# Performance work log

Hardware: AMD Instinct MI355X
Metric: run time of the kernel (lower is better)

Reference implementation:

```python
import jax, jax.numpy as jnp
import numpy as np

IN_SIZE = 64
NUM_FEATURES = 32
NUM_HEADS = 8
EPS = 1e-5


def setup_inputs() -> dict:
    key = jax.random.key(0)
    ks = jax.random.split(key, 12)
    D, F, Hh = IN_SIZE, NUM_FEATURES, NUM_HEADS
    M = Hh * F  # MLP width = num_heads * num_features
    s = 0.05
    return {
        "x": jax.random.normal(ks[0], (2, D, 48, 48), dtype=jnp.float32),
        # stacked per-head projection weights, stored [in, out]
        "Wq": jax.random.normal(ks[1], (Hh, D, F), dtype=jnp.float32) * s,
        "bq": jax.random.normal(ks[2], (Hh, F), dtype=jnp.float32) * s,
        "Wk": jax.random.normal(ks[3], (Hh, D, F), dtype=jnp.float32) * s,
        "bk": jax.random.normal(ks[4], (Hh, F), dtype=jnp.float32) * s,
        "Wv": jax.random.normal(ks[5], (Hh, D, F), dtype=jnp.float32) * s,
        "bv": jax.random.normal(ks[6], (Hh, F), dtype=jnp.float32) * s,
        "W1": jax.random.normal(ks[7], (M, M), dtype=jnp.float32) * s,
        "b1": jax.random.normal(ks[8], (M,), dtype=jnp.float32) * s,
        "W2": jax.random.normal(ks[9], (M, M), dtype=jnp.float32) * s,
        "b2": jax.random.normal(ks[10], (M,), dtype=jnp.float32) * s,
        "gamma": jnp.ones((M,), dtype=jnp.float32),
        "beta": jnp.zeros((M,), dtype=jnp.float32),
    }


def _inorm_lastdim(y):
    # InstanceNorm1d applied to channels-last tensor: normalizes LAST dim,
    # biased variance, eps=1e-5, no affine.
    mu = jnp.mean(y, axis=-1, keepdims=True)
    var = jnp.mean(jnp.square(y - mu), axis=-1, keepdims=True)
    return (y - mu) / jnp.sqrt(var + EPS)


def reference(x, Wq, bq, Wk, bk, Wv, bv, W1, b1, W2, b2, gamma, beta):
    N, D, H, W = x.shape
    F = NUM_FEATURES
    L = H * W
    flat = jnp.transpose(x, (0, 2, 3, 1)).reshape(N, L, D)  # [N, L, D]

    def proj(Wm, bm):  # Wm [Hh, D, F], bm [Hh, F] -> [Hh, N, L, F]
        y = jnp.einsum('nld,hdf->hnlf', flat, Wm) + bm[:, None, None, :]
        return jax.nn.relu(_inorm_lastdim(y))

    Q = proj(Wq, bq)
    K = proj(Wk, bk)
    V = proj(Wv, bv)

    scores = jnp.einsum('hnlf,hnmf->hnlm', Q, K) / jnp.sqrt(jnp.float32(F))
    # original: F.softmax(scaled) on 3D [N,L,L] -> legacy dim=1 (first L axis)
    att = jax.nn.softmax(scores, axis=2)
    A = jnp.einsum('hnlm,hnmf->hnlf', att, V)  # [Hh, N, L, F]

    heads = jnp.transpose(A, (1, 2, 0, 3)).reshape(N, L, NUM_HEADS * F)
    m = jax.nn.relu(heads @ W1 + b1)
    m = jax.nn.relu(m @ W2 + b2)
    o = _inorm_lastdim(m + heads)
    o = gamma * o + beta  # [N, L, Hh*F]
    return jnp.transpose(o, (0, 2, 1)).reshape(N, NUM_HEADS * F, H, W)
```

## Files before the change

### kernel.cpp

```cpp
#include <hip/hip_runtime.h>
#include <hip/hip_bf16.h>
#include <stdint.h>

#define L_TOT 2304
#define D_IN  64
#define NF    32
#define NH    8
#define NB    2
#define MW    256
#define CHS   4
#define NSTRIP (L_TOT/32)
#define RT    32

constexpr float EPSV  = 1e-5f;
constexpr float SCALE = 0.17677669529663687f;
constexpr float SHIFT = 20.0f;

typedef __bf16  bf16x8  __attribute__((ext_vector_type(8)));
typedef float   f32x16  __attribute__((ext_vector_type(16)));

union U32x4BF { uint32_t u[4]; bf16x8 v; };

static __device__ __forceinline__ uint32_t pack_bf16(float a, float b) {
    union { __bf16 h[2]; uint32_t u; } r;
    r.h[0] = (__bf16)a;
    r.h[1] = (__bf16)b;
    return r.u;
}

__global__ void k_prep(const float* __restrict__ W1, const float* __restrict__ W2,
                       __hip_bfloat16* __restrict__ W1t, __hip_bfloat16* __restrict__ W2t)
{
    const float* src = blockIdx.z ? W2 : W1;
    __hip_bfloat16* dst = blockIdx.z ? W2t : W1t;
    __shared__ float t[32][33];
    const int bi = blockIdx.x * 32, bj = blockIdx.y * 32;
    #pragma unroll
    for (int k = 0; k < 4; ++k)
        t[threadIdx.y + 8*k][threadIdx.x] = src[(size_t)(bi + threadIdx.y + 8*k) * MW + bj + threadIdx.x];
    __syncthreads();
    #pragma unroll
    for (int k = 0; k < 4; ++k)
        dst[(size_t)(bj + threadIdx.y + 8*k) * MW + bi + threadIdx.x] =
            __float2bfloat16(t[threadIdx.x][threadIdx.y + 8*k]);
}

__global__ __launch_bounds__(256) void k_prep2(
    const float* __restrict__ x,
    const float* __restrict__ Wq, const float* __restrict__ Wk, const float* __restrict__ Wv,
    __hip_bfloat16* __restrict__ xb, __hip_bfloat16* __restrict__ Wqkvt)
{
    const int job = blockIdx.x;
    const int tx = threadIdx.x & 31, ty = threadIdx.x >> 5;
    const float* src;
    size_t sstride;
    __hip_bfloat16* dst;
    if (job < 24) {
        int mtx = job >> 3, h = job & 7;
        const float* Wm = mtx == 0 ? Wq : (mtx == 1 ? Wk : Wv);
        src = Wm + (size_t)h * D_IN * NF;
        sstride = NF;
        dst = Wqkvt + (size_t)job * NF * D_IN;
    } else {
        int i = job - 24;
        int n = i / NSTRIP, lt = i % NSTRIP;
        src = x + (size_t)n * D_IN * L_TOT + lt * 32;
        sstride = L_TOT;
        dst = xb + ((size_t)n * L_TOT + lt * 32) * D_IN;
    }
    __shared__ float t[64][33];
    #pragma unroll
    for (int k = 0; k < 8; ++k)
        t[ty + 8 * k][tx] = src[(size_t)(ty + 8 * k) * sstride + tx];
    __syncthreads();
    #pragma unroll
    for (int k = 0; k < 4; ++k) {
        int col = ty + 8 * k;
        #pragma unroll
        for (int j = 0; j < 2; ++j)
            dst[(size_t)col * D_IN + tx + 32 * j] = __float2bfloat16(t[tx + 32 * j][col]);
    }
}

__global__ __launch_bounds__(256) void k_proj(
    const __hip_bfloat16* __restrict__ xb, const __hip_bfloat16* __restrict__ Wqkvt,
    const float* __restrict__ bq, const float* __restrict__ bk, const float* __restrict__ bv,
    __hip_bfloat16* __restrict__ Qo, __hip_bfloat16* __restrict__ Ko,
    __hip_bfloat16* __restrict__ Vt)
{
    const int ltile = blockIdx.x;
    const int n = blockIdx.y;
    const int h = blockIdx.z * 4 + (threadIdx.x >> 6);
    const int l0 = ltile * 32;
    const int lane = threadIdx.x & 63;
    const int c = lane & 31, hi = lane >> 5;
    const int hn = h * NB + n;

    const bf16x8* xp = reinterpret_cast<const bf16x8*>(
        xb + ((size_t)n * L_TOT + l0 + c) * D_IN);
    bf16x8 xf[4];
    #pragma unroll
    for (int t = 0; t < 4; ++t) xf[t] = xp[2 * t + hi];

    const float* bs[3] = {bq, bk, bv};

    #pragma unroll
    for (int mtx = 0; mtx < 3; ++mtx) {
        const bf16x8* wp = reinterpret_cast<const bf16x8*>(
            Wqkvt + ((size_t)(mtx * NH + h) * NF + c) * D_IN);
        f32x16 acc = {};
        #pragma unroll
        for (int t = 0; t < 4; ++t)
            acc = __builtin_amdgcn_mfma_f32_32x32x16_bf16(wp[2 * t + hi], xf[t], acc, 0, 0, 0);

        float bb[16];
        #pragma unroll
        for (int g = 0; g < 4; ++g) {
            float4 t4 = *reinterpret_cast<const float4*>(&bs[mtx][h * NF + 8 * g + 4 * hi]);
            bb[4 * g + 0] = t4.x; bb[4 * g + 1] = t4.y;
            bb[4 * g + 2] = t4.z; bb[4 * g + 3] = t4.w;
        }

        float v[16], s = 0.f, s2 = 0.f;
        #pragma unroll
        for (int r = 0; r < 16; ++r) {
            v[r] = acc[r] + bb[r];
            s += v[r]; s2 += v[r] * v[r];
        }
        s  += __shfl_xor(s, 32, 64);
        s2 += __shfl_xor(s2, 32, 64);
        float mu = s * (1.f / 32);
        float rstd = rsqrtf(s2 * (1.f / 32) - mu * mu + EPSV);
        float y[16];
        #pragma unroll
        for (int r = 0; r < 16; ++r) y[r] = fmaxf((v[r] - mu) * rstd, 0.f);

        if (mtx == 2) {
            #pragma unroll
            for (int r = 0; r < 16; ++r) {
                int f = (r & 3) + 8 * (r >> 2) + 4 * hi;
                Vt[((size_t)(hn * NSTRIP + ltile) * NF + f) * 32 + c] = __float2bfloat16(y[r]);
            }
        } else {
            if (mtx == 0) {
                #pragma unroll
                for (int r = 0; r < 16; ++r) y[r] *= SCALE;
            }
            uint32_t pk[8];
            #pragma unroll
            for (int q = 0; q < 8; ++q) pk[q] = pack_bf16(y[2 * q], y[2 * q + 1]);
            uint32_t rr[4];
            #pragma unroll
            for (int j = 0; j < 4; ++j)
                rr[j] = (uint32_t)__shfl_xor((int)(hi ? pk[j] : pk[4 + j]), 32, 64);
            uint32_t row[8];
            if (hi == 0) {
                row[0] = pk[0]; row[1] = pk[1]; row[2] = rr[0]; row[3] = rr[1];
                row[4] = pk[2]; row[5] = pk[3]; row[6] = rr[2]; row[7] = rr[3];
            } else {
                row[0] = rr[0]; row[1] = rr[1]; row[2] = pk[4]; row[3] = pk[5];
                row[4] = rr[2]; row[5] = rr[3]; row[6] = pk[6]; row[7] = pk[7];
            }
            __hip_bfloat16* dst = (mtx == 0 ? Qo : Ko)
                + ((size_t)hn * L_TOT + l0 + c) * NF + hi * 16;
            reinterpret_cast<uint4*>(dst)[0] = make_uint4(row[0], row[1], row[2], row[3]);
            reinterpret_cast<uint4*>(dst)[1] = make_uint4(row[4], row[5], row[6], row[7]);
        }
    }
}

__global__ __launch_bounds__(256) void k_stats(
    const __hip_bfloat16* __restrict__ Qb, const __hip_bfloat16* __restrict__ Kb,
    float* __restrict__ zpart)
{
    const int w = threadIdx.x >> 6;
    const int strip = blockIdx.x * 4 + w;
    const int hn = blockIdx.y;
    const int chunk = blockIdx.z;
    const int lane = threadIdx.x & 63;
    const int c = lane & 31, hi = lane >> 5;

    const bf16x8* kp = reinterpret_cast<const bf16x8*>(
        Kb + ((size_t)hn * L_TOT + strip * 32 + c) * NF);
    const bf16x8 ka0 = kp[hi];
    const bf16x8 ka1 = kp[2 + hi];

    float Zr[16];
    #pragma unroll
    for (int r = 0; r < 16; ++r) Zr[r] = 0.f;

    for (int it = 0; it < (L_TOT / 32) / CHS; ++it) {
        const int l0 = (chunk * ((L_TOT / 32) / CHS) + it) * 32;
        const bf16x8* qp = reinterpret_cast<const bf16x8*>(
            Qb + ((size_t)hn * L_TOT + l0 + c) * NF);
        bf16x8 qb0 = qp[hi];
        bf16x8 qb1 = qp[2 + hi];
        f32x16 s16 = {};
        s16 = __builtin_amdgcn_mfma_f32_32x32x16_bf16(ka0, qb0, s16, 0, 0, 0);
        s16 = __builtin_amdgcn_mfma_f32_32x32x16_bf16(ka1, qb1, s16, 0, 0, 0);
        #pragma unroll
        for (int r = 0; r < 16; ++r) Zr[r] += __expf(s16[r] - SHIFT);
    }
    #pragma unroll
    for (int r = 0; r < 16; ++r) {
        #pragma unroll
        for (int o = 16; o >= 1; o >>= 1) Zr[r] += __shfl_xor(Zr[r], o, 64);
    }
    if (c == 0) {
        float4* zp = reinterpret_cast<float4*>(
            zpart + ((size_t)chunk * 16 + hn) * L_TOT + strip * 32 + hi * 16);
        zp[0] = make_float4(Zr[0], Zr[1], Zr[2], Zr[3]);
        zp[1] = make_float4(Zr[4], Zr[5], Zr[6], Zr[7]);
        zp[2] = make_float4(Zr[8], Zr[9], Zr[10], Zr[11]);
        zp[3] = make_float4(Zr[12], Zr[13], Zr[14], Zr[15]);
    }
}

__global__ __launch_bounds__(256) void k_finish(
    const float* __restrict__ zpart, float* __restrict__ lse_p)
{
    const int idx = blockIdx.x * 256 + threadIdx.x;
    float Z = 0.f;
    #pragma unroll
    for (int cc = 0; cc < CHS; ++cc) Z += zpart[(size_t)cc * 16 * L_TOT + idx];
    lse_p[idx] = SHIFT + logf(Z);
}

__global__ __launch_bounds__(256) void k_apply(
    const __hip_bfloat16* __restrict__ Qb, const __hip_bfloat16* __restrict__ Kb,
    const __hip_bfloat16* __restrict__ Vt, const float* __restrict__ lse_p,
    float* __restrict__ partA)
{
    const int w = threadIdx.x >> 6;
    const int ltile = blockIdx.x;
    const int l0 = ltile * 32;
    const int hn = blockIdx.y;
    const int lane = threadIdx.x & 63;
    const int c = lane & 31, hi = lane >> 5;

    const bf16x8* qp = reinterpret_cast<const bf16x8*>(
        Qb + ((size_t)hn * L_TOT + l0 + c) * NF);
    const bf16x8 qb0 = qp[hi];
    const bf16x8 qb1 = qp[2 + hi];

    f32x16 acc = {};

    #pragma unroll 2
    for (int it = 0; it < NSTRIP / 4; ++it) {
        const int st = w * (NSTRIP / 4) + it;
        const bf16x8* kp = reinterpret_cast<const bf16x8*>(
            Kb + ((size_t)hn * L_TOT + st * 32 + c) * NF);
        f32x16 s16 = {};
        s16 = __builtin_amdgcn_mfma_f32_32x32x16_bf16(kp[hi], qb0, s16, 0, 0, 0);
        s16 = __builtin_amdgcn_mfma_f32_32x32x16_bf16(kp[2 + hi], qb1, s16, 0, 0, 0);

        const float4* lp = reinterpret_cast<const float4*>(
            lse_p + (size_t)hn * L_TOT + st * 32 + hi * 16);
        float lv[16];
        #pragma unroll
        for (int q = 0; q < 4; ++q) {
            float4 t = lp[q];
            lv[4 * q + 0] = t.x; lv[4 * q + 1] = t.y;
            lv[4 * q + 2] = t.z; lv[4 * q + 3] = t.w;
        }
        float p[16];
        #pragma unroll
        for (int r = 0; r < 16; ++r) p[r] = __expf(s16[r] - lv[r]);

        uint32_t wp[8];
        #pragma unroll
        for (int q = 0; q < 8; ++q) wp[q] = pack_bf16(p[2 * q], p[2 * q + 1]);

        uint32_t sendA = hi ? wp[0] : wp[2];
        uint32_t sendB = hi ? wp[1] : wp[3];
        uint32_t rA = (uint32_t)__shfl_xor((int)sendA, 32, 64);
        uint32_t rB = (uint32_t)__shfl_xor((int)sendB, 32, 64);
        U32x4BF fragP0;
        fragP0.u[0] = hi ? rA    : wp[0];
        fragP0.u[1] = hi ? rB    : wp[1];
        fragP0.u[2] = hi ? wp[2] : rA;
        fragP0.u[3] = hi ? wp[3] : rB;
        uint32_t sendC = hi ? wp[4] : wp[6];
        uint32_t sendD = hi ? wp[5] : wp[7];
        uint32_t rC = (uint32_t)__shfl_xor((int)sendC, 32, 64);
        uint32_t rD = (uint32_t)__shfl_xor((int)sendD, 32, 64);
        U32x4BF fragP1;
        fragP1.u[0] = hi ? rC    : wp[4];
        fragP1.u[1] = hi ? rD    : wp[5];
        fragP1.u[2] = hi ? wp[6] : rC;
        fragP1.u[3] = hi ? wp[7] : rD;

        const bf16x8* vp = reinterpret_cast<const bf16x8*>(
            Vt + ((size_t)(hn * NSTRIP + st) * NF + c) * 32);
        acc = __builtin_amdgcn_mfma_f32_32x32x16_bf16(fragP0.v, vp[hi], acc, 0, 0, 0);
        acc = __builtin_amdgcn_mfma_f32_32x32x16_bf16(fragP1.v, vp[2 + hi], acc, 0, 0, 0);
    }

    __shared__ float red[4][16][64];
    #pragma unroll
    for (int r = 0; r < 16; ++r) red[w][r][lane] = acc[r];
    __syncthreads();

    const int n = hn & 1, h = hn >> 1;
    float* outp = partA + ((size_t)(n * L_TOT + l0)) * MW + h * NF + c;
    #pragma unroll
    for (int j = 0; j < 4; ++j) {
        const int r = 4 * w + j;
        float sv = red[0][r][lane] + red[1][r][lane] + red[2][r][lane] + red[3][r][lane];
        const int row = (r & 3) + 8 * (r >> 2) + 4 * hi;
        outp[(size_t)row * MW] = sv;
    }
}

__global__ __launch_bounds__(512) void k_mlp(
    const float* __restrict__ partA,
    const __hip_bfloat16* __restrict__ W1t, const float* __restrict__ b1,
    const __hip_bfloat16* __restrict__ W2t, const float* __restrict__ b2,
    const float* __restrict__ gamma, const float* __restrict__ beta,
    float* __restrict__ out)
{
    const int blk = blockIdx.x;
    const int n  = blk / (L_TOT / RT);
    const int l0 = (blk % (L_TOT / RT)) * RT;
    const int tid = threadIdx.x;
    const int w = tid >> 6, lane = tid & 63;
    const int c = lane & 31, hi = lane >> 5;
    const int n0 = w * 32;

    __shared__ __align__(16) char smem[67584];
    float (*hsf)[MW] = reinterpret_cast<float (*)[MW]>(smem);
    __hip_bfloat16 (*hA)[264]  = reinterpret_cast<__hip_bfloat16 (*)[264]>(smem + 32768);
    __hip_bfloat16 (*msb)[264] = reinterpret_cast<__hip_bfloat16 (*)[264]>(smem + 49664);
    float (*ys)[MW] = reinterpret_cast<float (*)[MW]>(smem + 32768);
    float (*rs)[4]  = reinterpret_cast<float (*)[4]>(smem + 66560);
    float (*rs2)[4] = reinterpret_cast<float (*)[4]>(smem + 67072);

    for (int idx = tid; idx < RT * MW; idx += 512) {
        int r = idx >> 8, i = idx & 255;
        float v = partA[((size_t)n * L_TOT + l0 + r) * MW + i];
        hsf[r][i] = v;
        hA[r][i] = __float2bfloat16(v);
    }
    __syncthreads();

    const float bb1 = b1[n0 + c];
    bf16x8 B1[16];
    #pragma unroll
    for (int k0 = 0; k0 < 16; ++k0)
        B1[k0] = *reinterpret_cast<const bf16x8*>(W1t + (size_t)(n0 + c) * MW + k0 * 16 + hi * 8);
    f32x16 acc = {};
    #pragma unroll
    for (int k0 = 0; k0 < 16; ++k0) {
        bf16x8 a = *reinterpret_cast<const bf16x8*>(&hA[c][k0 * 16 + hi * 8]);
        acc = __builtin_amdgcn_mfma_f32_32x32x16_bf16(a, B1[k0], acc, 0, 0, 0);
    }
    #pragma unroll
    for (int r = 0; r < 16; ++r) {
        int row = (r & 3) + 8 * (r >> 2) + 4 * hi;
        msb[row][n0 + c] = __float2bfloat16(fmaxf(acc[r] + bb1, 0.f));
    }
    __syncthreads();

    const float bb2 = b2[n0 + c];
    bf16x8 B2[16];
    #pragma unroll
    for (int k0 = 0; k0 < 16; ++k0)
        B2[k0] = *reinterpret_cast<const bf16x8*>(W2t + (size_t)(n0 + c) * MW + k0 * 16 + hi * 8);
    f32x16 acc2 = {};
    #pragma unroll
    for (int k0 = 0; k0 < 16; ++k0) {
        bf16x8 a = *reinterpret_cast<const bf16x8*>(&msb[c][k0 * 16 + hi * 8]);
        acc2 = __builtin_amdgcn_mfma_f32_32x32x16_bf16(a, B2[k0], acc2, 0, 0, 0);
    }
    float yv[16];
    #pragma unroll
    for (int r = 0; r < 16; ++r) {
        int row = (r & 3) + 8 * (r >> 2) + 4 * hi;
        yv[r] = fmaxf(acc2[r] + bb2, 0.f) + hsf[row][n0 + c];
    }
    __syncthreads();
    #pragma unroll
    for (int r = 0; r < 16; ++r) {
        int row = (r & 3) + 8 * (r >> 2) + 4 * hi;
        ys[row][n0 + c] = yv[r];
    }
    __syncthreads();

    const int col = tid & 255;
    const int half = tid >> 8;
    const int wid = (tid >> 6) & 3;
    float vv[16];
    #pragma unroll
    for (int r = 0; r < 16; ++r) {
        float v = ys[half * 16 + r][col];
        vv[r] = v;
        float s = v, s2 = v * v;
        #pragma unroll
        for (int o = 32; o >= 1; o >>= 1) { s += __shfl_xor(s, o, 64); s2 += __shfl_xor(s2, o, 64); }
        if (lane == 0) { rs[half * 16 + r][wid] = s; rs2[half * 16 + r][wid] = s2; }
    }
    __syncthreads();
    const float g = gamma[col], be = beta[col];
    float ov[16];
    #pragma unroll
    for (int r = 0; r < 16; ++r) {
        int row = half * 16 + r;
        float s  = rs[row][0]  + rs[row][1]  + rs[row][2]  + rs[row][3];
        float s2 = rs2[row][0] + rs2[row][1] + rs2[row][2] + rs2[row][3];
        float mu  = s  * (1.f / MW);
        float var = s2 * (1.f / MW) - mu * mu;
        ov[r] = g * ((vv[r] - mu) * rsqrtf(var + EPSV)) + be;
    }
    float* ob = out + ((size_t)n * MW + col) * L_TOT + l0 + half * 16;
    #pragma unroll
    for (int q = 0; q < 4; ++q)
        reinterpret_cast<float4*>(ob)[q] =
            make_float4(ov[4 * q], ov[4 * q + 1], ov[4 * q + 2], ov[4 * q + 3]);
}

extern "C" void kernel_launch(void* const* d_in, const int* in_sizes, int n_in,
                              void* d_out, int out_size, void* d_ws, size_t ws_size,
                              hipStream_t stream) {
    const float* x  = (const float*)d_in[0];
    const float* Wq = (const float*)d_in[1];
    const float* bq = (const float*)d_in[2];
    const float* Wk = (const float*)d_in[3];
    const float* bk = (const float*)d_in[4];
    const float* Wv = (const float*)d_in[5];
    const float* bv = (const float*)d_in[6];
    const float* W1 = (const float*)d_in[7];
    const float* b1 = (const float*)d_in[8];
    const float* W2 = (const float*)d_in[9];
    const float* b2 = (const float*)d_in[10];
    const float* gm = (const float*)d_in[11];
    const float* bt = (const float*)d_in[12];
    float* out = (float*)d_out;

    const size_t QKVE = (size_t)16 * L_TOT * NF;
    const size_t XBE  = (size_t)NB * L_TOT * D_IN;
    const size_t WQE  = (size_t)3 * NH * NF * D_IN;
    const size_t WTE  = (size_t)MW * MW;
    const size_t ZN = (size_t)CHS * 16 * L_TOT;
    const size_t LN = (size_t)16 * L_TOT;

    __hip_bfloat16* Qb = (__hip_bfloat16*)d_ws;
    __hip_bfloat16* Kb = Qb + QKVE;
    __hip_bfloat16* Vt = Kb + QKVE;
    __hip_bfloat16* xb = Vt + QKVE;
    __hip_bfloat16* Wqkvt = xb + XBE;
    __hip_bfloat16* W1t = Wqkvt + WQE;
    __hip_bfloat16* W2t = W1t + WTE;
    float* zpart = (float*)(W2t + WTE);
    float* lse_p = zpart + ZN;
    float* partA = lse_p + LN;

    k_prep<<<dim3(8, 8, 2), dim3(32, 8), 0, stream>>>(W1, W2, W1t, W2t);
    k_prep2<<<dim3(24 + NB * NSTRIP), dim3(256), 0, stream>>>(x, Wq, Wk, Wv, xb, Wqkvt);
    k_proj<<<dim3(NSTRIP, NB, 2), dim3(256), 0, stream>>>(
        xb, Wqkvt, bq, bk, bv, Qb, Kb, Vt);
    k_stats<<<dim3(NSTRIP / 4, 16, CHS), dim3(256), 0, stream>>>(Qb, Kb, zpart);
    k_finish<<<dim3(16 * L_TOT / 256), dim3(256), 0, stream>>>(zpart, lse_p);
    k_apply<<<dim3(NSTRIP, 16), dim3(256), 0, stream>>>(
        Qb, Kb, Vt, lse_p, partA);
    k_mlp<<<dim3(NB * (L_TOT / RT)), dim3(512), 0, stream>>>(
        partA, W1t, b1, W2t, b2, gm, bt, out);
}
```

Measured before the change: 131.7 us.

## Fold softmax normalizer into V and use exp2 with prescaled Q

The softmax normalizer 1/Z is folded into V through a new small k_vscale kernel, so k_apply no longer loads log-sum-exp values or subtracts them per score. log2(e) is folded into the Q scale so both passes can use exp2f, and the fixed exponent shift is dropped. The apply kernel now runs 8 waves per block instead of 4, and the stats pass uses 8 chunks instead of 4. The cost is one extra launch, bf16 rounding of the rescaled V, and a possible exp2 overflow if scores ever grow large, since the shift is gone.

```diff
diff --git a/kernel.cpp b/kernel.cpp
--- a/kernel.cpp
+++ b/kernel.cpp
@@ -8,13 +8,12 @@
 #define NH    8
 #define NB    2
 #define MW    256
-#define CHS   4
+#define CHS   8
 #define NSTRIP (L_TOT/32)
 #define RT    32
 
 constexpr float EPSV  = 1e-5f;
-constexpr float SCALE = 0.17677669529663687f;
-constexpr float SHIFT = 20.0f;
+constexpr float SCALE2 = 0.2550351f;
 
 typedef __bf16  bf16x8  __attribute__((ext_vector_type(8)));
 typedef float   f32x16  __attribute__((ext_vector_type(16)));
@@ -144,7 +143,7 @@
         } else {
             if (mtx == 0) {
                 #pragma unroll
-                for (int r = 0; r < 16; ++r) y[r] *= SCALE;
+                for (int r = 0; r < 16; ++r) y[r] *= SCALE2;
             }
             uint32_t pk[8];
             #pragma unroll
@@ -199,7 +198,7 @@
         s16 = __builtin_amdgcn_mfma_f32_32x32x16_bf16(ka0, qb0, s16, 0, 0, 0);
         s16 = __builtin_amdgcn_mfma_f32_32x32x16_bf16(ka1, qb1, s16, 0, 0, 0);
         #pragma unroll
-        for (int r = 0; r < 16; ++r) Zr[r] += __expf(s16[r] - SHIFT);
+        for (int r = 0; r < 16; ++r) Zr[r] += exp2f(s16[r]);
     }
     #pragma unroll
     for (int r = 0; r < 16; ++r) {
@@ -217,18 +216,40 @@
 }
 
 __global__ __launch_bounds__(256) void k_finish(
-    const float* __restrict__ zpart, float* __restrict__ lse_p)
+    const float* __restrict__ zpart, float* __restrict__ zinv)
 {
     const int idx = blockIdx.x * 256 + threadIdx.x;
     float Z = 0.f;
     #pragma unroll
     for (int cc = 0; cc < CHS; ++cc) Z += zpart[(size_t)cc * 16 * L_TOT + idx];
-    lse_p[idx] = SHIFT + logf(Z);
-}
-
-__global__ __launch_bounds__(256) void k_apply(
+    const int p = idx & 31;
+    const int hi = (p >> 4) & 1, r = p & 15;
+    const int m_local = (r & 3) + 8 * (r >> 2) + 4 * hi;
+    zinv[(idx & ~31) + m_local] = 1.f / Z;
+}
+
+__global__ __launch_bounds__(256) void k_vscale(
+    __hip_bfloat16* __restrict__ Vt, const float* __restrict__ zinv)
+{
+    const int strip = blockIdx.x, hn = blockIdx.y;
+    const int f = threadIdx.x >> 3, mg = (threadIdx.x & 7) * 4;
+    const float4 zl = *reinterpret_cast<const float4*>(
+        zinv + (size_t)hn * L_TOT + strip * 32 + mg);
+    __hip_bfloat16* p = Vt + ((size_t)(hn * NSTRIP + strip) * NF + f) * 32 + mg;
+    uint2* p2 = reinterpret_cast<uint2*>(p);
+    uint2 old = *p2;
+    union { uint2 u2; __bf16 h[4]; } in, outv;
+    in.u2 = old;
+    outv.h[0] = (__bf16)((float)in.h[0] * zl.x);
+    outv.h[1] = (__bf16)((float)in.h[1] * zl.y);
+    outv.h[2] = (__bf16)((float)in.h[2] * zl.z);
+    outv.h[3] = (__bf16)((float)in.h[3] * zl.w);
+    *p2 = outv.u2;
+}
+
+__global__ __launch_bounds__(512) void k_apply(
     const __hip_bfloat16* __restrict__ Qb, const __hip_bfloat16* __restrict__ Kb,
-    const __hip_bfloat16* __restrict__ Vt, const float* __restrict__ lse_p,
+    const __hip_bfloat16* __restrict__ Vt,
     float* __restrict__ partA)
 {
     const int w = threadIdx.x >> 6;
@@ -245,27 +266,18 @@
 
     f32x16 acc = {};
 
-    #pragma unroll 2
-    for (int it = 0; it < NSTRIP / 4; ++it) {
-        const int st = w * (NSTRIP / 4) + it;
+    #pragma unroll 3
+    for (int it = 0; it < NSTRIP / 8; ++it) {
+        const int st = w * (NSTRIP / 8) + it;
         const bf16x8* kp = reinterpret_cast<const bf16x8*>(
             Kb + ((size_t)hn * L_TOT + st * 32 + c) * NF);
         f32x16 s16 = {};
         s16 = __builtin_amdgcn_mfma_f32_32x32x16_bf16(kp[hi], qb0, s16, 0, 0, 0);
         s16 = __builtin_amdgcn_mfma_f32_32x32x16_bf16(kp[2 + hi], qb1, s16, 0, 0, 0);
 
-        const float4* lp = reinterpret_cast<const float4*>(
-            lse_p + (size_t)hn * L_TOT + st * 32 + hi * 16);
-        float lv[16];
-        #pragma unroll
-        for (int q = 0; q < 4; ++q) {
-            float4 t = lp[q];
-            lv[4 * q + 0] = t.x; lv[4 * q + 1] = t.y;
-            lv[4 * q + 2] = t.z; lv[4 * q + 3] = t.w;
-        }
         float p[16];
         #pragma unroll
-        for (int r = 0; r < 16; ++r) p[r] = __expf(s16[r] - lv[r]);
+        for (int r = 0; r < 16; ++r) p[r] = exp2f(s16[r]);
 
         uint32_t wp[8];
         #pragma unroll
@@ -296,7 +308,7 @@
         acc = __builtin_amdgcn_mfma_f32_32x32x16_bf16(fragP1.v, vp[2 + hi], acc, 0, 0, 0);
     }
 
-    __shared__ float red[4][16][64];
+    __shared__ float red[8][16][64];
     #pragma unroll
     for (int r = 0; r < 16; ++r) red[w][r][lane] = acc[r];
     __syncthreads();
@@ -304,9 +316,11 @@
     const int n = hn & 1, h = hn >> 1;
     float* outp = partA + ((size_t)(n * L_TOT + l0)) * MW + h * NF + c;
     #pragma unroll
-    for (int j = 0; j < 4; ++j) {
-        const int r = 4 * w + j;
-        float sv = red[0][r][lane] + red[1][r][lane] + red[2][r][lane] + red[3][r][lane];
+    for (int j = 0; j < 2; ++j) {
+        const int r = 2 * w + j;
+        float sv = 0.f;
+        #pragma unroll
+        for (int k = 0; k < 8; ++k) sv += red[k][r][lane];
         const int row = (r & 3) + 8 * (r >> 2) + 4 * hi;
         outp[(size_t)row * MW] = sv;
     }
@@ -451,17 +465,17 @@
     __hip_bfloat16* W1t = Wqkvt + WQE;
     __hip_bfloat16* W2t = W1t + WTE;
     float* zpart = (float*)(W2t + WTE);
-    float* lse_p = zpart + ZN;
-    float* partA = lse_p + LN;
+    float* zinv  = zpart + ZN;
+    float* partA = zinv + LN;
 
     k_prep<<<dim3(8, 8, 2), dim3(32, 8), 0, stream>>>(W1, W2, W1t, W2t);
     k_prep2<<<dim3(24 + NB * NSTRIP), dim3(256), 0, stream>>>(x, Wq, Wk, Wv, xb, Wqkvt);
     k_proj<<<dim3(NSTRIP, NB, 2), dim3(256), 0, stream>>>(
         xb, Wqkvt, bq, bk, bv, Qb, Kb, Vt);
     k_stats<<<dim3(NSTRIP / 4, 16, CHS), dim3(256), 0, stream>>>(Qb, Kb, zpart);
-    k_finish<<<dim3(16 * L_TOT / 256), dim3(256), 0, stream>>>(zpart, lse_p);
-    k_apply<<<dim3(NSTRIP, 16), dim3(256), 0, stream>>>(
-        Qb, Kb, Vt, lse_p, partA);
+    k_finish<<<dim3(16 * L_TOT / 256), dim3(256), 0, stream>>>(zpart, zinv);
+    k_vscale<<<dim3(NSTRIP, 16), dim3(256), 0, stream>>>(Vt, zinv);
+    k_apply<<<dim3(NSTRIP, 16), dim3(512), 0, stream>>>(Qb, Kb, Vt, partA);
     k_mlp<<<dim3(NB * (L_TOT / RT)), dim3(512), 0, stream>>>(
         partA, W1t, b1, W2t, b2, gm, bt, out);
 }
```

Result: faster. 122.9 us (-6.6%).
